# Kernel tuning notes

Measured on AMD Instinct MI355X. Metric: run time of the kernel, lower is better.

The kernel has to match this reference:

```python
import jax, jax.numpy as jnp
import numpy as np

H = 8
D_MODEL = 512
D_K = D_MODEL // H
NEG = -1e9


def setup_inputs() -> dict:
    key = jax.random.key(0)
    ks = jax.random.split(key, 12)
    N, Lq, Lk = 2, 4096, 4096
    inp = {
        "query": jax.random.normal(ks[0], (N, Lq, D_MODEL), dtype=jnp.float32),
        "key": jax.random.normal(ks[1], (N, Lk, D_MODEL), dtype=jnp.float32),
        "value": jax.random.normal(ks[2], (N, Lk, D_MODEL), dtype=jnp.float32),
        "mask": jnp.ones((N, 1, Lk), dtype=jnp.int32),
    }
    scale = 0.02
    for i, nm in enumerate(["q", "k", "v", "o"]):
        inp[f"W{nm}"] = scale * jax.random.normal(ks[3 + i], (D_MODEL, D_MODEL), dtype=jnp.float32)
        inp[f"b{nm}"] = jnp.zeros((D_MODEL,), dtype=jnp.float32)
    return inp


def reference(query, key, value, mask, Wq, bq, Wk, bk, Wv, bv, Wo, bo):
    # torch Linear: y = x @ W.T + b
    N, Lq, _ = query.shape
    Lk = key.shape[1]
    q = (query @ Wq.T + bq).reshape(N, Lq, H, D_K)   # (N,Lq,h,dk)
    k = (key @ Wk.T + bk).reshape(N, Lk, H, D_K)     # (N,Lk,h,dk)
    v = (value @ Wv.T + bv).reshape(N, Lk, H, D_K)   # (N,Lk,h,dk)
    # scores: (N,h,Lq,Lk)
    scores = jnp.einsum("bqhd,bkhd->bhqk", q, k) / jnp.sqrt(jnp.float32(D_K))
    # mask (N,1,Lk) or (N,Lq,Lk) -> broadcast over heads (and Lq if singleton)
    m = mask[:, None, :, :]  # (N,1,1|Lq,Lk)
    scores = jnp.where(m == 0, jnp.float32(NEG), scores)
    attn = jax.nn.softmax(scores, axis=-1)
    # dropout is identity in eval mode (deterministic reference)
    out = jnp.einsum("bhqk,bkhd->bqhd", attn, v).reshape(N, Lq, D_MODEL)
    return out @ Wo.T + bo
```

## Files before the change

### kernel.cpp

```cpp
#include <hip/hip_runtime.h>
#include <hip/hip_bf16.h>

#define H 8
#define DM 512
#define DK 64
#define LSEQ 4096
#define NB 2
#define NSPLIT 2
#define KSPAN (LSEQ / NSPLIT)
#define NIT (KSPAN / 64)

#define QSCALE 0.18033688011112042f

typedef float f32x4 __attribute__((ext_vector_type(4)));
typedef __bf16 bf16x8 __attribute__((ext_vector_type(8)));
typedef __bf16 bf16x2 __attribute__((ext_vector_type(2)));
typedef unsigned short u16;

__device__ __forceinline__ u16 f2bf(float f) {
    union { float f; unsigned u; } v{f};
    return (u16)((v.u + 0x8000u) >> 16);
}

__device__ __forceinline__ unsigned pkbf(float a, float b) {
#if __has_builtin(__builtin_amdgcn_cvt_pk_bf16_f32)
    union { bf16x2 v; unsigned u; } x;
    x.v = __builtin_amdgcn_cvt_pk_bf16_f32(a, b);
    return x.u;
#else
    union { float f; unsigned u; } x{a}, y{b};
    return ((x.u + 0x8000u) >> 16) | ((y.u + 0x8000u) & 0xffff0000u);
#endif
}

__device__ __forceinline__ ushort4 cvt4(float4 a) {
    union { ushort4 s; uint2 u; } o;
    o.u.x = pkbf(a.x, a.y);
    o.u.y = pkbf(a.z, a.w);
    return o.s;
}

__device__ __forceinline__ float2 ubf2(unsigned u) {
    union { float f; unsigned v; } a, b;
    a.v = u << 16;
    b.v = u & 0xffff0000u;
    return make_float2(a.f, b.f);
}

__device__ __forceinline__ float fexp2(float x) {
#if __has_builtin(__builtin_amdgcn_exp2f)
    return __builtin_amdgcn_exp2f(x);
#else
    return exp2f(x);
#endif
}

__device__ __forceinline__ f32x4 mfma32(bf16x8 a, bf16x8 b, f32x4 c) {
    return __builtin_amdgcn_mfma_f32_16x16x32_bf16(a, b, c, 0, 0, 0);
}

__launch_bounds__(256, 2)
__global__ void proj_qkv(const float* __restrict__ Xq, const float* __restrict__ Xk,
                         const float* __restrict__ Xv,
                         const float* __restrict__ Wq, const float* __restrict__ Wk,
                         const float* __restrict__ Wv,
                         const float* __restrict__ bq, const float* __restrict__ bk,
                         const float* __restrict__ bv,
                         const int* __restrict__ mask,
                         u16* __restrict__ qo, u16* __restrict__ ko, u16* __restrict__ vo)
{
    const int mode = blockIdx.z;
    const float* X    = (mode == 0) ? Xq : (mode == 1) ? Xk : Xv;
    const float* W    = (mode == 0) ? Wq : (mode == 1) ? Wk : Wv;
    const float* bias = (mode == 0) ? bq : (mode == 1) ? bk : bv;
    u16* out          = (mode == 0) ? qo : (mode == 1) ? ko : vo;

    __shared__ __align__(16) u16 As[2][128][72];
    __shared__ __align__(16) u16 Bs[2][128][72];

    const int tid  = threadIdx.x;
    const int wave = tid >> 6;
    const int lane = tid & 63;
    const int g    = lane >> 4;
    const int ln   = lane & 15;
    const int wr   = wave >> 1;
    const int wc   = wave & 1;

    const int m0 = blockIdx.x * 128;
    const int n0 = blockIdx.y * 128;

    float4 xa[8], wb[8];
    #pragma unroll
    for (int i = 0; i < 8; ++i) {
        int idx = tid + 256 * i;
        int row = idx >> 4;
        int col = (idx & 15) * 4;
        xa[i] = *(const float4*)(X + (size_t)(m0 + row) * DM + col);
        wb[i] = *(const float4*)(W + (size_t)(n0 + row) * DM + col);
    }
    #pragma unroll
    for (int i = 0; i < 8; ++i) {
        int idx = tid + 256 * i;
        int row = idx >> 4;
        int col = (idx & 15) * 4;
        *(ushort4*)&As[0][row][col] = cvt4(xa[i]);
        *(ushort4*)&Bs[0][row][col] = cvt4(wb[i]);
    }

    f32x4 acc[4][4] = {};

    for (int kt = 0; kt < 8; ++kt) {
        const int cur = kt & 1;
        __syncthreads();

        if (kt < 7) {
            int kb = (kt + 1) * 64;
            #pragma unroll
            for (int i = 0; i < 8; ++i) {
                int idx = tid + 256 * i;
                int row = idx >> 4;
                int col = (idx & 15) * 4;
                xa[i] = *(const float4*)(X + (size_t)(m0 + row) * DM + kb + col);
                wb[i] = *(const float4*)(W + (size_t)(n0 + row) * DM + kb + col);
            }
        }

        bf16x8 af[4][2], bf[4][2];
        #pragma unroll
        for (int t = 0; t < 4; ++t) {
            af[t][0] = *(const bf16x8*)&As[cur][wr * 64 + t * 16 + ln][g * 8];
            af[t][1] = *(const bf16x8*)&As[cur][wr * 64 + t * 16 + ln][32 + g * 8];
            bf[t][0] = *(const bf16x8*)&Bs[cur][wc * 64 + t * 16 + ln][g * 8];
            bf[t][1] = *(const bf16x8*)&Bs[cur][wc * 64 + t * 16 + ln][32 + g * 8];
        }
        #pragma unroll
        for (int mt = 0; mt < 4; ++mt)
            #pragma unroll
            for (int nt = 0; nt < 4; ++nt) {
                acc[mt][nt] = mfma32(af[mt][0], bf[nt][0], acc[mt][nt]);
                acc[mt][nt] = mfma32(af[mt][1], bf[nt][1], acc[mt][nt]);
            }

        if (kt < 7) {
            int nxt = 1 - cur;
            #pragma unroll
            for (int i = 0; i < 8; ++i) {
                int idx = tid + 256 * i;
                int row = idx >> 4;
                int col = (idx & 15) * 4;
                *(ushort4*)&As[nxt][row][col] = cvt4(xa[i]);
                *(ushort4*)&Bs[nxt][row][col] = cvt4(wb[i]);
            }
        }
    }

    if (mode != 2) {
        #pragma unroll
        for (int nt = 0; nt < 4; ++nt) {
            int n  = n0 + wc * 64 + nt * 16 + ln;
            float bias_n = bias[n];
            int hh = n >> 6;
            int d  = n & (DK - 1);
            #pragma unroll
            for (int mt = 0; mt < 4; ++mt)
                #pragma unroll
                for (int r = 0; r < 4; ++r) {
                    int m  = m0 + wr * 64 + mt * 16 + g * 4 + r;
                    int bb = m >> 12;
                    int s  = m & (LSEQ - 1);
                    float val = acc[mt][nt][r] + bias_n;
                    if (mode == 0) val *= QSCALE;
                    else           val = mask[bb * LSEQ + s] ? val : 0.0f;
                    out[(size_t)((bb * H + hh) * LSEQ + s) * DK + d] = f2bf(val);
                }
        }
    } else {
        __syncthreads();
        u16* Ts = &As[0][0][0];
        const int bb = m0 >> 12;
        const int s0 = m0 & (LSEQ - 1);
        #pragma unroll
        for (int nt = 0; nt < 4; ++nt) {
            int dl = wc * 64 + nt * 16 + ln;
            float bias_n = bias[n0 + dl];
            #pragma unroll
            for (int mt = 0; mt < 4; ++mt)
                #pragma unroll
                for (int r = 0; r < 4; ++r) {
                    int sl = wr * 64 + mt * 16 + g * 4 + r;
                    float val = acc[mt][nt][r] + bias_n;
                    val = mask[bb * LSEQ + s0 + sl] ? val : 0.0f;
                    Ts[dl * 136 + sl] = f2bf(val);
                }
        }
        __syncthreads();
        int dl   = tid >> 1;
        int half = tid & 1;
        int n  = n0 + dl;
        int hh = n >> 6;
        int d  = n & (DK - 1);
        int sb = s0 + half * 64;
        u16* dst = out + ((size_t)((bb * H + hh) * DK + d) * LSEQ + sb);
        const u16* srcp = Ts + dl * 136 + half * 64;
        #pragma unroll
        for (int i = 0; i < 8; ++i)
            *(uint4*)(dst + i * 8) = *(const uint4*)(srcp + i * 8);
    }
}

__launch_bounds__(256, 4)
__global__ void flash(const u16* __restrict__ qws, const u16* __restrict__ kws,
                      const u16* __restrict__ vws, const int* __restrict__ mask,
                      u16* __restrict__ Opart, float* __restrict__ lpart)
{
    __shared__ u16 Ks[2][64][64];
    __shared__ u16 Vs[2][64][64];

    const int tid   = threadIdx.x;
    const int wave  = tid >> 6;
    const int lane  = tid & 63;
    const int g     = lane >> 4;
    const int ln    = lane & 15;
    const int b     = blockIdx.z;
    const int h     = blockIdx.y;
    const int qblk  = blockIdx.x & 31;
    const int split = blockIdx.x >> 5;
    const int q0    = qblk * 128;
    const int kstart = split * KSPAN;

    const u16* qp = qws + ((size_t)((b * H + h) * LSEQ) + q0 + wave * 32 + ln) * DK;
    const u16* kp = kws + (size_t)(b * H + h) * LSEQ * DK;
    const u16* vp = vws + (size_t)(b * H + h) * DK * LSEQ;
    const int* mp = mask + b * LSEQ;

    int nmask = 0;
    for (int t = 0; t < NIT; ++t) {
        int mval = mp[kstart + t * 64 + lane];
        unsigned long long bal = __ballot(mval == 0);
        nmask += (int)__popcll(bal);
    }
    const float fnmask = (float)nmask;

    bf16x8 qf[2][2];
    qf[0][0] = *(const bf16x8*)(qp + g * 8);
    qf[0][1] = *(const bf16x8*)(qp + 32 + g * 8);
    qf[1][0] = *(const bf16x8*)(qp + 16 * DK + g * 8);
    qf[1][1] = *(const bf16x8*)(qp + 16 * DK + 32 + g * 8);

    union OU { unsigned u[4]; bf16x8 v; } onesu;
    onesu.u[0] = onesu.u[1] = onesu.u[2] = onesu.u[3] = 0x3F803F80u;
    const bf16x8 vones = onesu.v;

    f32x4 accO[2][4] = {};
    f32x4 accL[2] = {};

    const int row = tid >> 3;
    const int c   = tid & 7;
    const int swz = row & 7;
    const int kcol = (c ^ swz) * 8;
    const int vcol0 = ((2 * c) & 3) * 16 + (c >> 1) * 4;
    const int vs0 = vcol0 >> 3;
    const int vof = vcol0 & 7;
    const int vw0 = ((vs0 ^ swz) * 8) + vof;
    const int vw1 = (((vs0 + 2) ^ swz) * 8) + vof;
    const int rs = ln & 7;

    uint4 kr0, kr1, vr0, vr1;
    kr0 = *(const uint4*)(kp + (size_t)(kstart + row) * DK + c * 8);
    kr1 = *(const uint4*)(kp + (size_t)(kstart + row + 32) * DK + c * 8);
    vr0 = *(const uint4*)(vp + (size_t)row * LSEQ + kstart + c * 8);
    vr1 = *(const uint4*)(vp + (size_t)(row + 32) * LSEQ + kstart + c * 8);
    *(uint4*)&Ks[0][row][kcol]      = kr0;
    *(uint4*)&Ks[0][row + 32][kcol] = kr1;
    *(uint2*)&Vs[0][row][vw0]       = make_uint2(vr0.x, vr0.y);
    *(uint2*)&Vs[0][row][vw1]       = make_uint2(vr0.z, vr0.w);
    *(uint2*)&Vs[0][row + 32][vw0]  = make_uint2(vr1.x, vr1.y);
    *(uint2*)&Vs[0][row + 32][vw1]  = make_uint2(vr1.z, vr1.w);

    for (int it = 0; it < NIT; ++it) {
        const int cur = it & 1;
        __syncthreads();

        if (it < NIT - 1) {
            int kn = kstart + it * 64 + 64;
            kr0 = *(const uint4*)(kp + (size_t)(kn + row) * DK + c * 8);
            kr1 = *(const uint4*)(kp + (size_t)(kn + row + 32) * DK + c * 8);
            vr0 = *(const uint4*)(vp + (size_t)row * LSEQ + kn + c * 8);
            vr1 = *(const uint4*)(vp + (size_t)(row + 32) * LSEQ + kn + c * 8);
        }

        __builtin_amdgcn_s_setprio(1);
        f32x4 sc[2][4];
        #pragma unroll
        for (int kb = 0; kb < 4; ++kb) {
            bf16x8 kf0 = *(const bf16x8*)&Ks[cur][kb * 16 + ln][(g ^ rs) * 8];
            bf16x8 kf1 = *(const bf16x8*)&Ks[cur][kb * 16 + ln][((g + 4) ^ rs) * 8];
            #pragma unroll
            for (int j = 0; j < 2; ++j) {
                f32x4 z = {};
                z = mfma32(kf0, qf[j][0], z);
                z = mfma32(kf1, qf[j][1], z);
                sc[j][kb] = z;
            }
        }
        __builtin_amdgcn_s_setprio(0);

        #pragma unroll
        for (int kb = 0; kb < 4; ++kb)
            #pragma unroll
            for (int j = 0; j < 2; ++j) {
                sc[j][kb][0] = fexp2(sc[j][kb][0]);
                sc[j][kb][1] = fexp2(sc[j][kb][1]);
                sc[j][kb][2] = fexp2(sc[j][kb][2]);
                sc[j][kb][3] = fexp2(sc[j][kb][3]);
            }

        union PU { unsigned u[4]; bf16x8 v; } p01[2], p23[2];
        #pragma unroll
        for (int j = 0; j < 2; ++j) {
            p01[j].u[0] = pkbf(sc[j][0][0], sc[j][0][1]);
            p01[j].u[1] = pkbf(sc[j][0][2], sc[j][0][3]);
            p01[j].u[2] = pkbf(sc[j][1][0], sc[j][1][1]);
            p01[j].u[3] = pkbf(sc[j][1][2], sc[j][1][3]);
            p23[j].u[0] = pkbf(sc[j][2][0], sc[j][2][1]);
            p23[j].u[1] = pkbf(sc[j][2][2], sc[j][2][3]);
            p23[j].u[2] = pkbf(sc[j][3][0], sc[j][3][1]);
            p23[j].u[3] = pkbf(sc[j][3][2], sc[j][3][3]);
        }

        __builtin_amdgcn_s_setprio(1);
        #pragma unroll
        for (int j = 0; j < 2; ++j) {
            accL[j] = mfma32(p01[j].v, vones, accL[j]);
            accL[j] = mfma32(p23[j].v, vones, accL[j]);
        }
        #pragma unroll
        for (int t = 0; t < 4; ++t) {
            bf16x8 vb01 = *(const bf16x8*)&Vs[cur][t * 16 + ln][((2 * g) ^ rs) * 8];
            bf16x8 vb23 = *(const bf16x8*)&Vs[cur][t * 16 + ln][((2 * g + 1) ^ rs) * 8];
            #pragma unroll
            for (int j = 0; j < 2; ++j) {
                accO[j][t] = mfma32(p01[j].v, vb01, accO[j][t]);
                accO[j][t] = mfma32(p23[j].v, vb23, accO[j][t]);
            }
        }
        __builtin_amdgcn_s_setprio(0);

        if (it < NIT - 1) {
            int nxt = 1 - cur;
            *(uint4*)&Ks[nxt][row][kcol]      = kr0;
            *(uint4*)&Ks[nxt][row + 32][kcol] = kr1;
            *(uint2*)&Vs[nxt][row][vw0]       = make_uint2(vr0.x, vr0.y);
            *(uint2*)&Vs[nxt][row][vw1]       = make_uint2(vr0.z, vr0.w);
            *(uint2*)&Vs[nxt][row + 32][vw0]  = make_uint2(vr1.x, vr1.y);
            *(uint2*)&Vs[nxt][row + 32][vw1]  = make_uint2(vr1.z, vr1.w);
        }
    }

    const size_t PLANE = (size_t)NB * LSEQ * DM;
    u16* opp = Opart + (size_t)split * PLANE;

    #pragma unroll
    for (int j = 0; j < 2; ++j) {
        if (ln == 0) {
            #pragma unroll
            for (int r = 0; r < 4; ++r)
                lpart[(size_t)split * (NB * H * LSEQ) + ((size_t)(b * H + h) * LSEQ)
                      + q0 + wave * 32 + j * 16 + g * 4 + r] = accL[j][r] - fnmask;
        }
        #pragma unroll
        for (int r = 0; r < 4; ++r) {
            float linv = 1.0f / (accL[j][r] - fnmask);
            size_t base = ((size_t)(b * LSEQ) + q0 + wave * 32 + j * 16 + g * 4 + r) * DM + h * DK;
            #pragma unroll
            for (int t = 0; t < 4; ++t)
                opp[base + t * 16 + ln] = f2bf(accO[j][t][r] * linv);
        }
    }
}

__launch_bounds__(256, 4)
__global__ void reduce_split(const u16* __restrict__ Opart, const float* __restrict__ lpart,
                             u16* __restrict__ ows)
{
    const size_t PLANE = (size_t)NB * LSEQ * DM;
    size_t gid  = (size_t)blockIdx.x * 256 + threadIdx.x;
    size_t flat = gid * 8;

    int b   = (int)(flat >> 21);
    int rem = (int)(flat & ((1 << 21) - 1));
    int q   = rem >> 9;
    int hh  = (rem & 511) >> 6;
    size_t lidx = ((size_t)(b * H + hh) * LSEQ) + q;

    float l0 = lpart[lidx];
    float l1 = lpart[(size_t)NB * H * LSEQ + lidx];
    float inv = 1.0f / (l0 + l1);
    float w0 = l0 * inv, w1 = l1 * inv;

    uint4 c0 = *(const uint4*)(Opart + flat);
    uint4 c1 = *(const uint4*)(Opart + PLANE + flat);

    float o[8];
    {
        float2 a, bv;
        a = ubf2(c0.x); bv = ubf2(c1.x); o[0] = w0 * a.x + w1 * bv.x; o[1] = w0 * a.y + w1 * bv.y;
        a = ubf2(c0.y); bv = ubf2(c1.y); o[2] = w0 * a.x + w1 * bv.x; o[3] = w0 * a.y + w1 * bv.y;
        a = ubf2(c0.z); bv = ubf2(c1.z); o[4] = w0 * a.x + w1 * bv.x; o[5] = w0 * a.y + w1 * bv.y;
        a = ubf2(c0.w); bv = ubf2(c1.w); o[6] = w0 * a.x + w1 * bv.x; o[7] = w0 * a.y + w1 * bv.y;
    }
    uint4 r;
    r.x = pkbf(o[0], o[1]);
    r.y = pkbf(o[2], o[3]);
    r.z = pkbf(o[4], o[5]);
    r.w = pkbf(o[6], o[7]);
    *(uint4*)(ows + flat) = r;
}

__launch_bounds__(256, 3)
__global__ void proj_out(const u16* __restrict__ A, const float* __restrict__ Wo,
                         const float* __restrict__ bo, float* __restrict__ out)
{
    __shared__ __align__(16) u16 As[2][128][68];
    __shared__ __align__(16) u16 Bs[2][64][68];

    const int tid  = threadIdx.x;
    const int wave = tid >> 6;
    const int lane = tid & 63;
    const int g    = lane >> 4;
    const int ln   = lane & 15;

    const int m0 = blockIdx.x * 128;
    const int n0 = blockIdx.y * 64;

    uint4 aa[4];
    float4 wb[4];
    #pragma unroll
    for (int i = 0; i < 4; ++i) {
        int idx = tid + 256 * i;
        int row = idx >> 3;
        int col = (idx & 7) * 8;
        aa[i] = *(const uint4*)(A + (size_t)(m0 + row) * DM + col);
        int rwb = idx >> 4;
        int cwb = (idx & 15) * 4;
        wb[i] = *(const float4*)(Wo + (size_t)(n0 + rwb) * DM + cwb);
    }
    #pragma unroll
    for (int i = 0; i < 4; ++i) {
        int idx = tid + 256 * i;
        int row = idx >> 3;
        int col = (idx & 7) * 8;
        *(uint4*)&As[0][row][col] = aa[i];
        int rwb = idx >> 4;
        int cwb = (idx & 15) * 4;
        *(ushort4*)&Bs[0][rwb][cwb] = cvt4(wb[i]);
    }

    f32x4 acc[2][4] = {};

    for (int kt = 0; kt < 8; ++kt) {
        const int cur = kt & 1;
        __syncthreads();

        if (kt < 7) {
            int kb = (kt + 1) * 64;
            #pragma unroll
            for (int i = 0; i < 4; ++i) {
                int idx = tid + 256 * i;
                int row = idx >> 3;
                int col = (idx & 7) * 8;
                aa[i] = *(const uint4*)(A + (size_t)(m0 + row) * DM + kb + col);
                int rwb = idx >> 4;
                int cwb = (idx & 15) * 4;
                wb[i] = *(const float4*)(Wo + (size_t)(n0 + rwb) * DM + kb + cwb);
            }
        }

        bf16x8 af[2][2], bf[4][2];
        #pragma unroll
        for (int mt = 0; mt < 2; ++mt) {
            af[mt][0] = *(const bf16x8*)&As[cur][wave * 32 + mt * 16 + ln][g * 8];
            af[mt][1] = *(const bf16x8*)&As[cur][wave * 32 + mt * 16 + ln][32 + g * 8];
        }
        #pragma unroll
        for (int nt = 0; nt < 4; ++nt) {
            bf[nt][0] = *(const bf16x8*)&Bs[cur][nt * 16 + ln][g * 8];
            bf[nt][1] = *(const bf16x8*)&Bs[cur][nt * 16 + ln][32 + g * 8];
        }
        #pragma unroll
        for (int mt = 0; mt < 2; ++mt)
            #pragma unroll
            for (int nt = 0; nt < 4; ++nt) {
                acc[mt][nt] = mfma32(af[mt][0], bf[nt][0], acc[mt][nt]);
                acc[mt][nt] = mfma32(af[mt][1], bf[nt][1], acc[mt][nt]);
            }

        if (kt < 7) {
            int nxt = 1 - cur;
            #pragma unroll
            for (int i = 0; i < 4; ++i) {
                int idx = tid + 256 * i;
                int row = idx >> 3;
                int col = (idx & 7) * 8;
                *(uint4*)&As[nxt][row][col] = aa[i];
                int rwb = idx >> 4;
                int cwb = (idx & 15) * 4;
                *(ushort4*)&Bs[nxt][rwb][cwb] = cvt4(wb[i]);
            }
        }
    }

    #pragma unroll
    for (int nt = 0; nt < 4; ++nt) {
        int n = n0 + nt * 16 + ln;
        float bias_n = bo[n];
        #pragma unroll
        for (int mt = 0; mt < 2; ++mt)
            #pragma unroll
            for (int r = 0; r < 4; ++r) {
                int m = m0 + wave * 32 + mt * 16 + g * 4 + r;
                out[(size_t)m * DM + n] = acc[mt][nt][r] + bias_n;
            }
    }
}

extern "C" void kernel_launch(void* const* d_in, const int* in_sizes, int n_in,
                              void* d_out, int out_size, void* d_ws, size_t ws_size,
                              hipStream_t stream) {
    (void)in_sizes; (void)n_in; (void)out_size; (void)ws_size;

    const float* query = (const float*)d_in[0];
    const float* key   = (const float*)d_in[1];
    const float* value = (const float*)d_in[2];
    const int*   mask  = (const int*)d_in[3];
    const float* Wq = (const float*)d_in[4];
    const float* bq = (const float*)d_in[5];
    const float* Wk = (const float*)d_in[6];
    const float* bk = (const float*)d_in[7];
    const float* Wv = (const float*)d_in[8];
    const float* bv = (const float*)d_in[9];
    const float* Wo = (const float*)d_in[10];
    const float* bo = (const float*)d_in[11];
    float* out = (float*)d_out;

    const size_t PLANE = (size_t)NB * H * LSEQ * DK;
    u16* qws   = (u16*)d_ws;
    u16* kws   = qws + PLANE;
    u16* vws   = kws + PLANE;
    u16* ows   = vws + PLANE;
    u16* Opart = ows + PLANE;
    float* lpart = (float*)(Opart + (size_t)NSPLIT * PLANE);

    dim3 blk(256);
    proj_qkv<<<dim3(64, 4, 3), blk, 0, stream>>>(query, key, value, Wq, Wk, Wv,
                                                 bq, bk, bv, mask, qws, kws, vws);
    flash<<<dim3(32 * NSPLIT, H, NB), blk, 0, stream>>>(qws, kws, vws, mask, Opart, lpart);
    reduce_split<<<dim3(2048), blk, 0, stream>>>(Opart, lpart, ows);
    proj_out<<<dim3(64, 8, 1), blk, 0, stream>>>(ows, Wo, bo, out);
}
```

Baseline: 232.6 us.

## Software-pipeline flash loop: overlap next-tile QK/exp with current PV MFMAs

Restructures the attention inner loop so the scores and exponentials for tile i are computed while the PV product still uses the probabilities from tile i-1. This needs a prologue, an epilogue, and triple-buffered V in shared memory. The aim is to let the exp and pack VALU work interleave with the PV MFMAs instead of running as a serial dependency chain. The LDS stores are moved to the top of the loop and the s_setprio hints are dropped. It costs extra registers and LDS, which may reduce occupancy below the launch bound of four blocks.

```diff
diff --git a/kernel.cpp b/kernel.cpp
--- a/kernel.cpp
+++ b/kernel.cpp
@@ -214,7 +214,7 @@
                       u16* __restrict__ Opart, float* __restrict__ lpart)
 {
     __shared__ u16 Ks[2][64][64];
-    __shared__ u16 Vs[2][64][64];
+    __shared__ u16 Vs[3][64][64];
 
     const int tid   = threadIdx.x;
     const int wave  = tid >> 6;
@@ -276,25 +276,24 @@
     *(uint2*)&Vs[0][row][vw1]       = make_uint2(vr0.z, vr0.w);
     *(uint2*)&Vs[0][row + 32][vw0]  = make_uint2(vr1.x, vr1.y);
     *(uint2*)&Vs[0][row + 32][vw1]  = make_uint2(vr1.z, vr1.w);
-
-    for (int it = 0; it < NIT; ++it) {
-        const int cur = it & 1;
-        __syncthreads();
-
-        if (it < NIT - 1) {
-            int kn = kstart + it * 64 + 64;
-            kr0 = *(const uint4*)(kp + (size_t)(kn + row) * DK + c * 8);
-            kr1 = *(const uint4*)(kp + (size_t)(kn + row + 32) * DK + c * 8);
-            vr0 = *(const uint4*)(vp + (size_t)row * LSEQ + kn + c * 8);
-            vr1 = *(const uint4*)(vp + (size_t)(row + 32) * LSEQ + kn + c * 8);
-        }
-
-        __builtin_amdgcn_s_setprio(1);
+    {
+        const int kn = kstart + 64;
+        kr0 = *(const uint4*)(kp + (size_t)(kn + row) * DK + c * 8);
+        kr1 = *(const uint4*)(kp + (size_t)(kn + row + 32) * DK + c * 8);
+        vr0 = *(const uint4*)(vp + (size_t)row * LSEQ + kn + c * 8);
+        vr1 = *(const uint4*)(vp + (size_t)(row + 32) * LSEQ + kn + c * 8);
+    }
+    __syncthreads();
+
+    union PU { unsigned u[4]; bf16x8 v; };
+    PU pp01[2], pp23[2];
+
+    {
         f32x4 sc[2][4];
         #pragma unroll
         for (int kb = 0; kb < 4; ++kb) {
-            bf16x8 kf0 = *(const bf16x8*)&Ks[cur][kb * 16 + ln][(g ^ rs) * 8];
-            bf16x8 kf1 = *(const bf16x8*)&Ks[cur][kb * 16 + ln][((g + 4) ^ rs) * 8];
+            bf16x8 kf0 = *(const bf16x8*)&Ks[0][kb * 16 + ln][(g ^ rs) * 8];
+            bf16x8 kf1 = *(const bf16x8*)&Ks[0][kb * 16 + ln][((g + 4) ^ rs) * 8];
             #pragma unroll
             for (int j = 0; j < 2; ++j) {
                 f32x4 z = {};
@@ -303,8 +302,6 @@
                 sc[j][kb] = z;
             }
         }
-        __builtin_amdgcn_s_setprio(0);
-
         #pragma unroll
         for (int kb = 0; kb < 4; ++kb)
             #pragma unroll
@@ -314,46 +311,114 @@
                 sc[j][kb][2] = fexp2(sc[j][kb][2]);
                 sc[j][kb][3] = fexp2(sc[j][kb][3]);
             }
-
-        union PU { unsigned u[4]; bf16x8 v; } p01[2], p23[2];
         #pragma unroll
         for (int j = 0; j < 2; ++j) {
-            p01[j].u[0] = pkbf(sc[j][0][0], sc[j][0][1]);
-            p01[j].u[1] = pkbf(sc[j][0][2], sc[j][0][3]);
-            p01[j].u[2] = pkbf(sc[j][1][0], sc[j][1][1]);
-            p01[j].u[3] = pkbf(sc[j][1][2], sc[j][1][3]);
-            p23[j].u[0] = pkbf(sc[j][2][0], sc[j][2][1]);
-            p23[j].u[1] = pkbf(sc[j][2][2], sc[j][2][3]);
-            p23[j].u[2] = pkbf(sc[j][3][0], sc[j][3][1]);
-            p23[j].u[3] = pkbf(sc[j][3][2], sc[j][3][3]);
-        }
-
-        __builtin_amdgcn_s_setprio(1);
+            pp01[j].u[0] = pkbf(sc[j][0][0], sc[j][0][1]);
+            pp01[j].u[1] = pkbf(sc[j][0][2], sc[j][0][3]);
+            pp01[j].u[2] = pkbf(sc[j][1][0], sc[j][1][1]);
+            pp01[j].u[3] = pkbf(sc[j][1][2], sc[j][1][3]);
+            pp23[j].u[0] = pkbf(sc[j][2][0], sc[j][2][1]);
+            pp23[j].u[1] = pkbf(sc[j][2][2], sc[j][2][3]);
+            pp23[j].u[2] = pkbf(sc[j][3][0], sc[j][3][1]);
+            pp23[j].u[3] = pkbf(sc[j][3][2], sc[j][3][3]);
+        }
+    }
+
+    int vwi = 1, vpi = 0;
+    for (int it = 1; it < NIT; ++it) {
+        const int kcur = it & 1;
+        u16 (*VsW)[64] = Vs[vwi];
+        u16 (*VsP)[64] = Vs[vpi];
+
+        *(uint4*)&Ks[kcur][row][kcol]      = kr0;
+        *(uint4*)&Ks[kcur][row + 32][kcol] = kr1;
+        *(uint2*)&VsW[row][vw0]       = make_uint2(vr0.x, vr0.y);
+        *(uint2*)&VsW[row][vw1]       = make_uint2(vr0.z, vr0.w);
+        *(uint2*)&VsW[row + 32][vw0]  = make_uint2(vr1.x, vr1.y);
+        *(uint2*)&VsW[row + 32][vw1]  = make_uint2(vr1.z, vr1.w);
+        __syncthreads();
+
+        if (it < NIT - 1) {
+            const int kn = kstart + (it + 1) * 64;
+            kr0 = *(const uint4*)(kp + (size_t)(kn + row) * DK + c * 8);
+            kr1 = *(const uint4*)(kp + (size_t)(kn + row + 32) * DK + c * 8);
+            vr0 = *(const uint4*)(vp + (size_t)row * LSEQ + kn + c * 8);
+            vr1 = *(const uint4*)(vp + (size_t)(row + 32) * LSEQ + kn + c * 8);
+        }
+
+        f32x4 sc[2][4];
+        #pragma unroll
+        for (int kb = 0; kb < 4; ++kb) {
+            bf16x8 kf0 = *(const bf16x8*)&Ks[kcur][kb * 16 + ln][(g ^ rs) * 8];
+            bf16x8 kf1 = *(const bf16x8*)&Ks[kcur][kb * 16 + ln][((g + 4) ^ rs) * 8];
+            #pragma unroll
+            for (int j = 0; j < 2; ++j) {
+                f32x4 z = {};
+                z = mfma32(kf0, qf[j][0], z);
+                z = mfma32(kf1, qf[j][1], z);
+                sc[j][kb] = z;
+            }
+        }
+
+        #pragma unroll
+        for (int kb = 0; kb < 4; ++kb)
+            #pragma unroll
+            for (int j = 0; j < 2; ++j) {
+                sc[j][kb][0] = fexp2(sc[j][kb][0]);
+                sc[j][kb][1] = fexp2(sc[j][kb][1]);
+                sc[j][kb][2] = fexp2(sc[j][kb][2]);
+                sc[j][kb][3] = fexp2(sc[j][kb][3]);
+            }
+        PU pn01[2], pn23[2];
         #pragma unroll
         for (int j = 0; j < 2; ++j) {
-            accL[j] = mfma32(p01[j].v, vones, accL[j]);
-            accL[j] = mfma32(p23[j].v, vones, accL[j]);
+            pn01[j].u[0] = pkbf(sc[j][0][0], sc[j][0][1]);
+            pn01[j].u[1] = pkbf(sc[j][0][2], sc[j][0][3]);
+            pn01[j].u[2] = pkbf(sc[j][1][0], sc[j][1][1]);
+            pn01[j].u[3] = pkbf(sc[j][1][2], sc[j][1][3]);
+            pn23[j].u[0] = pkbf(sc[j][2][0], sc[j][2][1]);
+            pn23[j].u[1] = pkbf(sc[j][2][2], sc[j][2][3]);
+            pn23[j].u[2] = pkbf(sc[j][3][0], sc[j][3][1]);
+            pn23[j].u[3] = pkbf(sc[j][3][2], sc[j][3][3]);
+        }
+
+        #pragma unroll
+        for (int j = 0; j < 2; ++j) {
+            accL[j] = mfma32(pp01[j].v, vones, accL[j]);
+            accL[j] = mfma32(pp23[j].v, vones, accL[j]);
         }
         #pragma unroll
         for (int t = 0; t < 4; ++t) {
-            bf16x8 vb01 = *(const bf16x8*)&Vs[cur][t * 16 + ln][((2 * g) ^ rs) * 8];
-            bf16x8 vb23 = *(const bf16x8*)&Vs[cur][t * 16 + ln][((2 * g + 1) ^ rs) * 8];
+            bf16x8 vb01 = *(const bf16x8*)&VsP[t * 16 + ln][((2 * g) ^ rs) * 8];
+            bf16x8 vb23 = *(const bf16x8*)&VsP[t * 16 + ln][((2 * g + 1) ^ rs) * 8];
             #pragma unroll
             for (int j = 0; j < 2; ++j) {
-                accO[j][t] = mfma32(p01[j].v, vb01, accO[j][t]);
-                accO[j][t] = mfma32(p23[j].v, vb23, accO[j][t]);
-            }
-        }
-        __builtin_amdgcn_s_setprio(0);
-
-        if (it < NIT - 1) {
-            int nxt = 1 - cur;
-            *(uint4*)&Ks[nxt][row][kcol]      = kr0;
-            *(uint4*)&Ks[nxt][row + 32][kcol] = kr1;
-            *(uint2*)&Vs[nxt][row][vw0]       = make_uint2(vr0.x, vr0.y);
-            *(uint2*)&Vs[nxt][row][vw1]       = make_uint2(vr0.z, vr0.w);
-            *(uint2*)&Vs[nxt][row + 32][vw0]  = make_uint2(vr1.x, vr1.y);
-            *(uint2*)&Vs[nxt][row + 32][vw1]  = make_uint2(vr1.z, vr1.w);
+                accO[j][t] = mfma32(pp01[j].v, vb01, accO[j][t]);
+                accO[j][t] = mfma32(pp23[j].v, vb23, accO[j][t]);
+            }
+        }
+
+        pp01[0] = pn01[0]; pp01[1] = pn01[1];
+        pp23[0] = pn23[0]; pp23[1] = pn23[1];
+        vpi = vwi; vwi = (vwi == 2) ? 0 : vwi + 1;
+    }
+
+    {
+        u16 (*VsP)[64] = Vs[vpi];
+        #pragma unroll
+        for (int j = 0; j < 2; ++j) {
+            accL[j] = mfma32(pp01[j].v, vones, accL[j]);
+            accL[j] = mfma32(pp23[j].v, vones, accL[j]);
+        }
+        #pragma unroll
+        for (int t = 0; t < 4; ++t) {
+            bf16x8 vb01 = *(const bf16x8*)&VsP[t * 16 + ln][((2 * g) ^ rs) * 8];
+            bf16x8 vb23 = *(const bf16x8*)&VsP[t * 16 + ln][((2 * g + 1) ^ rs) * 8];
+            #pragma unroll
+            for (int j = 0; j < 2; ++j) {
+                accO[j][t] = mfma32(pp01[j].v, vb01, accO[j][t]);
+                accO[j][t] = mfma32(pp23[j].v, vb23, accO[j][t]);
+            }
         }
     }
 
```

Result: slower. 241.8 us (+3.9%).
